# Optimization experiments

Measured on AMD Instinct MI355X. Metric: run time of the kernel, lower is better.

Reference implementation:

```python
import jax, jax.numpy as jnp
import numpy as np

B, C, K, D = 8192, 64, 256, 64  # batch, ncodebooks, ncentroids, subvect_len
BN_EPS = 1e-5


def setup_inputs() -> dict:
    key = jax.random.key(0)
    k1, k2 = jax.random.split(key)
    return {
        "inputs": jax.random.normal(k1, (B, C, D), dtype=jnp.float32),
        "centroids_k": jax.random.normal(k2, (C, K, D), dtype=jnp.float32) * 0.1,
        "bn_gamma": jnp.ones((C,), dtype=jnp.float32),
        "bn_beta": jnp.zeros((C,), dtype=jnp.float32),
    }


def _response(inputs, centroids_k, bn_gamma, bn_beta):
    # dot-metric scores: (B, C, K)
    r = jnp.einsum('bcd,ckd->bck', inputs, centroids_k)
    # BatchNorm1d over channel dim C (training mode: biased batch stats over B and K)
    mean = r.mean(axis=(0, 2), keepdims=True)
    var = ((r - mean) ** 2).mean(axis=(0, 2), keepdims=True)
    r = (r - mean) * jax.lax.rsqrt(var + BN_EPS)
    return r * bn_gamma[None, :, None] + bn_beta[None, :, None]


def reference(inputs, centroids_k, bn_gamma, bn_beta):
    r = _response(inputs, centroids_k, bn_gamma, bn_beta)
    # torch.max(response, -1) -> (values, indices)
    mse = r.max(axis=-1)                 # (B, C)
    codes = jnp.argmax(r, axis=-1)       # (B, C) int
    # tie_in_n_out=True: _centroids_v is _centroids_k
    return codes, mse, centroids_k
```

## Files before the change

kernel.cpp:

```cpp
#include <hip/hip_runtime.h>

#define B_  8192
#define C_  64
#define K_  256
#define D_  64
#define WROWS 64
#define GX  (B_ / (8 * WROWS))
#define BC_ (B_ * C_)
#define BN_EPS 1e-5

#define WCAP_C 1024
#define DELTA  2.5e-3f

typedef _Float16 f16x8 __attribute__((ext_vector_type(8)));
typedef float    f32x4 __attribute__((ext_vector_type(4)));

__device__ __forceinline__ int swz(int row, int dbyte) {
    return (row * 128 + dbyte) ^ ((row & 7) << 4);
}

__device__ __forceinline__ f16x8 cvt8(const float* p) {
    float4 u0 = *(const float4*)p;
    float4 u1 = *(const float4*)(p + 4);
    return (f16x8){(_Float16)u0.x, (_Float16)u0.y, (_Float16)u0.z, (_Float16)u0.w,
                   (_Float16)u1.x, (_Float16)u1.y, (_Float16)u1.z, (_Float16)u1.w};
}

#define MERGE2(B1, S1, B2, S2)                                              \
    {                                                                       \
        const float lo_ = fminf(B1, B2);                                    \
        B1 = fmaxf(B1, B2);                                                 \
        S1 = fmaxf(lo_, fmaxf(S1, S2));                                     \
    }

__global__ __launch_bounds__(256) void dpq_prep(
    const float* __restrict__ cent, float* __restrict__ csum,
    int* __restrict__ wcount)
{
    __shared__ float pacc[4][D_];
    const int c = blockIdx.x, t = threadIdx.x;
    const int d = t & 63, seg = t >> 6;
    const float* g = cent + (size_t)c * K_ * D_ + (size_t)seg * 64 * D_ + d;
    float s = 0.f;
#pragma unroll 8
    for (int k = 0; k < 64; ++k) s += g[(size_t)k * D_];
    pacc[seg][d] = s;
    __syncthreads();
    if (t < D_)
        csum[c * D_ + t] = (pacc[0][t] + pacc[1][t]) + (pacc[2][t] + pacc[3][t]);
    if (t == 0) wcount[c] = 0;
}

__global__ __launch_bounds__(512, 6) void dpq_mfma(
    const float* __restrict__ x,
    const float* __restrict__ cent,
    const float* __restrict__ gamma,
    const float* __restrict__ csum,
    float* __restrict__ ws_pk,
    float* __restrict__ part_sum,
    float* __restrict__ part_sq,
    int* __restrict__ wcount,
    int* __restrict__ worklist)
{
    __shared__ char lds[34816];
    const int lid = blockIdx.x + GX * blockIdx.y;
    const int c   = lid & 63;
    const int bxv = lid >> 6;
    const int tid = threadIdx.x;
    const float sgn = (gamma[c] < 0.0f) ? -1.0f : 1.0f;

    {
        const int row = tid >> 1, half = tid & 1;
        const float* g = cent + ((size_t)c * K_ + row) * D_ + half * 32;
#pragma unroll
        for (int q = 0; q < 4; ++q) {
            float v[8];
#pragma unroll
            for (int j = 0; j < 8; ++j) v[j] = g[q * 8 + j] * sgn;
            f16x8 h = {(_Float16)v[0], (_Float16)v[1], (_Float16)v[2], (_Float16)v[3],
                       (_Float16)v[4], (_Float16)v[5], (_Float16)v[6], (_Float16)v[7]};
            *(f16x8*)(lds + swz(row, half * 64 + q * 16)) = h;
        }
    }
    if (tid < 128) {
        const int row = tid >> 3, q = tid & 7;
        f16x8 h = {0, 0, 0, 0, 0, 0, 0, 0};
        if (row == 0) {
            const float* cs = csum + c * D_ + q * 8;
#pragma unroll
            for (int j = 0; j < 8; ++j) h[j] = (_Float16)(cs[j] * sgn);
        }
        *(f16x8*)(lds + 32768 + swz(row, q * 16)) = h;
    }
    __syncthreads();

    const int wid = tid >> 6, lane = tid & 63;
    const int col = lane & 15, grp = lane >> 4;
    const unsigned g4 = (unsigned)(grp * 4);
    const int b0 = bxv * (8 * WROWS) + wid * WROWS;

    f16x8 xfa[4], xfb[4];
    {
        const float* xb = x + ((size_t)(b0 + col) * C_ + c) * D_ + grp * 8;
        const size_t st16 = (size_t)16 * C_ * D_;
#pragma unroll
        for (int T = 0; T < 4; ++T) {
            xfa[T] = cvt8(xb + T * st16);
            xfb[T] = cvt8(xb + T * st16 + 32);
        }
    }

    float taccs[4] = {0.f, 0.f, 0.f, 0.f};
    float taccq[4] = {0.f, 0.f, 0.f, 0.f};
    float bestv[4], secv[4];
#pragma unroll
    for (int T = 0; T < 4; ++T) { bestv[T] = -3.4e38f; secv[T] = -3.4e38f; }

#pragma unroll 4
    for (int t = 0; t < 16; ++t) {
        const f16x8 a0 = *(const f16x8*)(lds + swz(t * 16 + col,      grp * 16));
        const f16x8 a1 = *(const f16x8*)(lds + swz(t * 16 + col, 64 + grp * 16));
        const unsigned kt = ((unsigned)t << 4) | g4;

        f32x4 p[4];
        __builtin_amdgcn_s_setprio(1);
#pragma unroll
        for (int T = 0; T < 4; ++T) {
            f32x4 acc = {0.f, 0.f, 0.f, 0.f};
            acc = __builtin_amdgcn_mfma_f32_16x16x32_f16(a0, xfa[T], acc, 0, 0, 0);
            acc = __builtin_amdgcn_mfma_f32_16x16x32_f16(a1, xfb[T], acc, 0, 0, 0);
            p[T] = acc;
        }
        __builtin_amdgcn_s_setprio(0);

#pragma unroll
        for (int j = 0; j < 4; ++j) {
            const unsigned kj = kt + j;
#pragma unroll
            for (int T = 0; T < 4; ++T) {
                const float r = p[T][j];
                taccq[T] = fmaf(r, r, taccq[T]);
                const float pk = __uint_as_float(
                    (__float_as_uint(r) & 0xFFFFFF00u) | kj);
                secv[T]  = __builtin_amdgcn_fmed3f(pk, bestv[T], secv[T]);
                bestv[T] = fmaxf(bestv[T], pk);
            }
        }
    }

    {
        const f16x8 a0v = *(const f16x8*)(lds + 32768 + swz(col,      grp * 16));
        const f16x8 a1v = *(const f16x8*)(lds + 32768 + swz(col, 64 + grp * 16));
#pragma unroll
        for (int T = 0; T < 4; ++T) {
            f32x4 pv = {0.f, 0.f, 0.f, 0.f};
            pv = __builtin_amdgcn_mfma_f32_16x16x32_f16(a0v, xfa[T], pv, 0, 0, 0);
            pv = __builtin_amdgcn_mfma_f32_16x16x32_f16(a1v, xfb[T], pv, 0, 0, 0);
            taccs[T] += pv[0];
        }
    }

#pragma unroll
    for (int T = 0; T < 4; ++T) {
        float bv = bestv[T], sv = secv[T];
#pragma unroll
        for (int m = 16; m <= 32; m <<= 1) {
            const float ob = __shfl_xor(bv, m);
            const float os = __shfl_xor(sv, m);
            MERGE2(bv, sv, ob, os);
        }
        if (grp == 0) {
            const int b = b0 + T * 16 + col;
            ws_pk[(size_t)c * B_ + b] = bv;
            if (bv - sv < DELTA) {
                const int slot = atomicAdd(&wcount[c], 1);
                if (slot < WCAP_C) worklist[c * WCAP_C + slot] = b;
            }
        }
    }

    float accs = (taccs[0] + taccs[1]) + (taccs[2] + taccs[3]);
    float accq = (taccq[0] + taccq[1]) + (taccq[2] + taccq[3]);
#pragma unroll
    for (int m = 1; m <= 32; m <<= 1) {
        accs += __shfl_xor(accs, m);
        accq += __shfl_xor(accq, m);
    }
    __syncthreads();
    float* red = (float*)lds;
    if (lane == 0) { red[wid] = accs; red[8 + wid] = accq; }
    __syncthreads();
    if (tid == 0) {
        float s = 0.f, q = 0.f;
#pragma unroll
        for (int w = 0; w < 8; ++w) { s += red[w]; q += red[8 + w]; }
        part_sum[c * GX + bxv] = s;
        part_sq [c * GX + bxv] = q;
    }
}

__global__ __launch_bounds__(256) void dpq_referee(
    const float* __restrict__ x,
    const float* __restrict__ cent,
    const float* __restrict__ gamma,
    const int* __restrict__ wcount,
    const int* __restrict__ worklist,
    float* __restrict__ ws_pk)
{
    __shared__ float cl[K_ * D_];
    const int c = blockIdx.x;
    int n = wcount[c];
    if (n > WCAP_C) n = WCAP_C;
    if (n <= 0) return;
    const int t = threadIdx.x;
    const float sgnf = (gamma[c] < 0.0f) ? -1.0f : 1.0f;

    {
        const float* g = cent + ((size_t)c * K_ + t) * D_;
#pragma unroll 8
        for (int d = 0; d < D_; ++d)
            cl[t * D_ + (d ^ (t & 31))] = g[d];
    }
    __syncthreads();

    const int wid = t >> 6, lane = t & 63;
    for (int i = blockIdx.y * 4 + wid; i < n; i += gridDim.y * 4) {
        const int b = worklist[c * WCAP_C + i];
        const float* xr = x + ((size_t)b * C_ + c) * D_;
        double bv = -1.0e300;
        int bk = 0;
#pragma unroll
        for (int q = 0; q < 4; ++q) {
            const int k = q * 64 + lane;
            const int sw = k & 31;
            double s = 0.0;
#pragma unroll 8
            for (int d = 0; d < D_; ++d)
                s += (double)xr[d] * (double)cl[k * D_ + (d ^ sw)];
            s *= (double)sgnf;
            if (s > bv) { bv = s; bk = k; }
        }
#pragma unroll
        for (int m = 1; m <= 32; m <<= 1) {
            const double ov = __shfl_xor(bv, m);
            const int   ok = __shfl_xor(bk, m);
            if (ov > bv || (ov == bv && ok < bk)) { bv = ov; bk = ok; }
        }
        if (lane == 0) {
            const unsigned bits =
                (__float_as_uint((float)bv) & 0xFFFFFF00u) | (unsigned)bk;
            ws_pk[(size_t)c * B_ + b] = __uint_as_float(bits);
        }
    }
}

__global__ __launch_bounds__(256) void dpq_apply(
    float* __restrict__ out,
    const float* __restrict__ ws_pk,
    const float* __restrict__ part_sum,
    const float* __restrict__ part_sq,
    const float* __restrict__ gamma,
    const float* __restrict__ beta,
    const float* __restrict__ cent)
{
    __shared__ float sc_s[C_], sh_s[C_];
    const int tid = threadIdx.x;
    if (tid < C_) {
        double s = 0.0, q = 0.0;
#pragma unroll
        for (int i = 0; i < GX; ++i) {
            s += (double)part_sum[tid * GX + i];
            q += (double)part_sq [tid * GX + i];
        }
        const double n    = (double)B_ * (double)K_;
        const double mean = s / n;
        const double var  = q / n - mean * mean;
        const double sc   = fabs((double)gamma[tid]) / sqrt(var + BN_EPS);
        sc_s[tid] = (float)sc;
        sh_s[tid] = (float)((double)beta[tid] - mean * sc);
    }
    __syncthreads();

    const int g = blockIdx.x * 256 + tid;
    const int c = g & (C_ - 1);
    const int b = g >> 6;
    const unsigned bits = __float_as_uint(ws_pk[(size_t)c * B_ + b]);
    const float raw = __uint_as_float(bits & 0xFFFFFF00u);
    const float sc = sc_s[c];
    const float sh = sh_s[c];
    if (sc == 0.0f) {
        out[g] = 0.0f;
        out[(size_t)BC_ + g] = sh;
    } else {
        out[g] = (float)(bits & 255u);
        out[(size_t)BC_ + g] = fmaf(raw, sc, sh);
    }

    if (g < (C_ * K_ * D_) / 4) {
        ((float4*)(out + 2 * (size_t)BC_))[g] = ((const float4*)cent)[g];
    }
}

extern "C" void kernel_launch(void* const* d_in, const int* in_sizes, int n_in,
                              void* d_out, int out_size, void* d_ws, size_t ws_size,
                              hipStream_t stream)
{
    const float* x     = (const float*)d_in[0];
    const float* cent  = (const float*)d_in[1];
    const float* gamma = (const float*)d_in[2];
    const float* beta  = (const float*)d_in[3];
    float* out = (float*)d_out;
    float* ws  = (float*)d_ws;

    float* csum     = ws;
    float* part_sum = ws + 4096;
    float* part_sq  = ws + 5120;
    int*   wcount   = (int*)(ws + 6144);
    int*   worklist = (int*)(ws + 6208);
    float* ws_pk    = ws + 71744;

    hipLaunchKernelGGL(dpq_prep, dim3(C_), dim3(256), 0, stream,
                       cent, csum, wcount);
    dim3 g1(GX, C_);
    hipLaunchKernelGGL(dpq_mfma, g1, dim3(512), 0, stream,
                       x, cent, gamma, csum, ws_pk, part_sum, part_sq,
                       wcount, worklist);
    hipLaunchKernelGGL(dpq_referee, dim3(C_, 4), dim3(256), 0, stream,
                       x, cent, gamma, wcount, worklist, ws_pk);
    hipLaunchKernelGGL(dpq_apply, dim3(BC_ / 256), dim3(256), 0, stream,
                       out, ws_pk, part_sum, part_sq, gamma, beta, cent);
}
```

Before: 100.2 us.

## Precompute swizzled fp16 centroid planes and DMA them directly into LDS

The prep kernel now converts each codebook's centroids once to sign-adjusted, swizzled fp16 planes in workspace. The main kernel loads those planes with global_load_lds instead of every block re-reading and converting fp32 centroids. The block shrinks to 256 threads (4 waves, 256 rows), which doubles the grid and so the number of plane loads per codebook. The row sum for the batch-norm mean is now accumulated from the scores directly rather than with an extra MFMA against the centroid sum, which removes the csum path.

```diff
diff --git a/kernel.cpp b/kernel.cpp
--- a/kernel.cpp
+++ b/kernel.cpp
@@ -5,7 +5,8 @@
 #define K_  256
 #define D_  64
 #define WROWS 64
-#define GX  (B_ / (8 * WROWS))
+#define BROWS 256
+#define GX  (B_ / BROWS)
 #define BC_ (B_ * C_)
 #define BN_EPS 1e-5
 
@@ -34,70 +35,57 @@
     }
 
 __global__ __launch_bounds__(256) void dpq_prep(
-    const float* __restrict__ cent, float* __restrict__ csum,
-    int* __restrict__ wcount)
-{
-    __shared__ float pacc[4][D_];
-    const int c = blockIdx.x, t = threadIdx.x;
-    const int d = t & 63, seg = t >> 6;
-    const float* g = cent + (size_t)c * K_ * D_ + (size_t)seg * 64 * D_ + d;
-    float s = 0.f;
-#pragma unroll 8
-    for (int k = 0; k < 64; ++k) s += g[(size_t)k * D_];
-    pacc[seg][d] = s;
-    __syncthreads();
-    if (t < D_)
-        csum[c * D_ + t] = (pacc[0][t] + pacc[1][t]) + (pacc[2][t] + pacc[3][t]);
-    if (t == 0) wcount[c] = 0;
-}
-
-__global__ __launch_bounds__(512, 6) void dpq_mfma(
+    const float* __restrict__ cent, const float* __restrict__ gamma,
+    char* __restrict__ planes, int* __restrict__ wcount)
+{
+    const int c = blockIdx.x, k = threadIdx.x;
+    const float sgn = (gamma[c] < 0.0f) ? -1.0f : 1.0f;
+    const float* g = cent + ((size_t)c * K_ + k) * D_;
+    char* pl = planes + (size_t)c * 32768;
+#pragma unroll
+    for (int q = 0; q < 8; ++q) {
+        float v[8];
+#pragma unroll
+        for (int j = 0; j < 8; ++j) v[j] = g[q * 8 + j] * sgn;
+        f16x8 h = {(_Float16)v[0], (_Float16)v[1], (_Float16)v[2], (_Float16)v[3],
+                   (_Float16)v[4], (_Float16)v[5], (_Float16)v[6], (_Float16)v[7]};
+        *(f16x8*)(pl + swz(k, q * 16)) = h;
+    }
+    if (k == 0) wcount[c] = 0;
+}
+
+__global__ __launch_bounds__(256, 5) void dpq_mfma(
     const float* __restrict__ x,
-    const float* __restrict__ cent,
-    const float* __restrict__ gamma,
-    const float* __restrict__ csum,
+    const char*  __restrict__ planes,
     float* __restrict__ ws_pk,
     float* __restrict__ part_sum,
     float* __restrict__ part_sq,
     int* __restrict__ wcount,
     int* __restrict__ worklist)
 {
-    __shared__ char lds[34816];
+    __shared__ char lds[32768];
     const int lid = blockIdx.x + GX * blockIdx.y;
     const int c   = lid & 63;
     const int bxv = lid >> 6;
     const int tid = threadIdx.x;
-    const float sgn = (gamma[c] < 0.0f) ? -1.0f : 1.0f;
+    const int wid = tid >> 6, lane = tid & 63;
 
     {
-        const int row = tid >> 1, half = tid & 1;
-        const float* g = cent + ((size_t)c * K_ + row) * D_ + half * 32;
-#pragma unroll
-        for (int q = 0; q < 4; ++q) {
-            float v[8];
-#pragma unroll
-            for (int j = 0; j < 8; ++j) v[j] = g[q * 8 + j] * sgn;
-            f16x8 h = {(_Float16)v[0], (_Float16)v[1], (_Float16)v[2], (_Float16)v[3],
-                       (_Float16)v[4], (_Float16)v[5], (_Float16)v[6], (_Float16)v[7]};
-            *(f16x8*)(lds + swz(row, half * 64 + q * 16)) = h;
-        }
-    }
-    if (tid < 128) {
-        const int row = tid >> 3, q = tid & 7;
-        f16x8 h = {0, 0, 0, 0, 0, 0, 0, 0};
-        if (row == 0) {
-            const float* cs = csum + c * D_ + q * 8;
-#pragma unroll
-            for (int j = 0; j < 8; ++j) h[j] = (_Float16)(cs[j] * sgn);
-        }
-        *(f16x8*)(lds + 32768 + swz(row, q * 16)) = h;
-    }
-    __syncthreads();
-
-    const int wid = tid >> 6, lane = tid & 63;
+        const char* pg = planes + (size_t)c * 32768;
+#pragma unroll
+        for (int i = 0; i < 8; ++i) {
+            const int off = (wid * 8 + i) * 1024;
+            __builtin_amdgcn_global_load_lds(
+                (const __attribute__((address_space(1))) unsigned int*)
+                    (pg + off + lane * 16),
+                (__attribute__((address_space(3))) unsigned int*)(lds + off),
+                16, 0, 0);
+        }
+    }
+
     const int col = lane & 15, grp = lane >> 4;
     const unsigned g4 = (unsigned)(grp * 4);
-    const int b0 = bxv * (8 * WROWS) + wid * WROWS;
+    const int b0 = bxv * BROWS + wid * WROWS;
 
     f16x8 xfa[4], xfb[4];
     {
@@ -109,6 +97,7 @@
             xfb[T] = cvt8(xb + T * st16 + 32);
         }
     }
+    __syncthreads();
 
     float taccs[4] = {0.f, 0.f, 0.f, 0.f};
     float taccq[4] = {0.f, 0.f, 0.f, 0.f};
@@ -139,24 +128,13 @@
 #pragma unroll
             for (int T = 0; T < 4; ++T) {
                 const float r = p[T][j];
+                taccs[T] += r;
                 taccq[T] = fmaf(r, r, taccq[T]);
                 const float pk = __uint_as_float(
                     (__float_as_uint(r) & 0xFFFFFF00u) | kj);
                 secv[T]  = __builtin_amdgcn_fmed3f(pk, bestv[T], secv[T]);
                 bestv[T] = fmaxf(bestv[T], pk);
             }
-        }
-    }
-
-    {
-        const f16x8 a0v = *(const f16x8*)(lds + 32768 + swz(col,      grp * 16));
-        const f16x8 a1v = *(const f16x8*)(lds + 32768 + swz(col, 64 + grp * 16));
-#pragma unroll
-        for (int T = 0; T < 4; ++T) {
-            f32x4 pv = {0.f, 0.f, 0.f, 0.f};
-            pv = __builtin_amdgcn_mfma_f32_16x16x32_f16(a0v, xfa[T], pv, 0, 0, 0);
-            pv = __builtin_amdgcn_mfma_f32_16x16x32_f16(a1v, xfb[T], pv, 0, 0, 0);
-            taccs[T] += pv[0];
         }
     }
 
@@ -188,14 +166,11 @@
     }
     __syncthreads();
     float* red = (float*)lds;
-    if (lane == 0) { red[wid] = accs; red[8 + wid] = accq; }
+    if (lane == 0) { red[wid] = accs; red[4 + wid] = accq; }
     __syncthreads();
     if (tid == 0) {
-        float s = 0.f, q = 0.f;
-#pragma unroll
-        for (int w = 0; w < 8; ++w) { s += red[w]; q += red[8 + w]; }
-        part_sum[c * GX + bxv] = s;
-        part_sq [c * GX + bxv] = q;
+        part_sum[c * GX + bxv] = (red[0] + red[1]) + (red[2] + red[3]);
+        part_sq [c * GX + bxv] = (red[4] + red[5]) + (red[6] + red[7]);
     }
 }
 
@@ -312,19 +287,18 @@
     float* out = (float*)d_out;
     float* ws  = (float*)d_ws;
 
-    float* csum     = ws;
-    float* part_sum = ws + 4096;
-    float* part_sq  = ws + 5120;
-    int*   wcount   = (int*)(ws + 6144);
-    int*   worklist = (int*)(ws + 6208);
-    float* ws_pk    = ws + 71744;
+    char*  planes   = (char*)ws;
+    float* part_sum = ws + 524288;
+    float* part_sq  = ws + 526336;
+    int*   wcount   = (int*)(ws + 528384);
+    int*   worklist = (int*)(ws + 528448);
+    float* ws_pk    = ws + 593984;
 
     hipLaunchKernelGGL(dpq_prep, dim3(C_), dim3(256), 0, stream,
-                       cent, csum, wcount);
+                       cent, gamma, planes, wcount);
     dim3 g1(GX, C_);
-    hipLaunchKernelGGL(dpq_mfma, g1, dim3(512), 0, stream,
-                       x, cent, gamma, csum, ws_pk, part_sum, part_sq,
-                       wcount, worklist);
+    hipLaunchKernelGGL(dpq_mfma, g1, dim3(256), 0, stream,
+                       x, planes, ws_pk, part_sum, part_sq, wcount, worklist);
     hipLaunchKernelGGL(dpq_referee, dim3(C_, 4), dim3(256), 0, stream,
                        x, cent, gamma, wcount, worklist, ws_pk);
     hipLaunchKernelGGL(dpq_apply, dim3(BC_ / 256), dim3(256), 0, stream,
```

After: 101.6 us. About the same (+1.4%).
